# Kernel tuning notes

Hardware: AMD Instinct MI355X
Metric: run time of the kernel (lower is better)

The kernel has to match this reference:

```python
import jax, jax.numpy as jnp
import numpy as np

N = 60000      # n_total_medical_code (graph nodes)
E = 600000     # nnz of sparse adjacency
D = 128        # args.dynamic_size
FEAT = 128     # args.feature_size
B = 256        # len(codeid)
P = 10000      # n_patient
ALPHA = 0.1
EPS = 1e-12    # F.normalize eps


def _l2norm(x):
    # F.normalize(x) : L2 over dim=1
    n = jnp.sqrt(jnp.sum(x * x, axis=1, keepdims=True))
    return x / jnp.maximum(n, EPS)


def _gcn_layer(x, W, edge_row, edge_col, edge_val, init_x):
    # support = X @ W ; out = A @ support (sparse) ; alpha-blend residual ; ReLU
    support = x @ W                                    # [N, D]
    msgs = support[edge_col] * edge_val[:, None]       # [E, D] gather + scale
    agg = jax.ops.segment_sum(msgs, edge_row, num_segments=N)  # [N, D] scatter-add
    out = ALPHA * agg + (1.0 - ALPHA) * init_x
    return jax.nn.relu(out)


def setup_inputs() -> dict:
    key = jax.random.key(0)
    ks = jax.random.split(key, 16)
    stdv = 1.0 / np.sqrt(D)
    in_rnn = D + 1 + FEAT  # 257
    stdv_rnn = 1.0 / np.sqrt(D)
    return {
        "code_dynamic": jax.random.normal(ks[0], (N, D), jnp.float32),
        "init_code_dynamic": jax.random.normal(ks[1], (N, D), jnp.float32),
        "patient_dynamic": jax.random.normal(ks[2], (P, D), jnp.float32),
        "timediffs": jax.random.normal(ks[3], (B, 1), jnp.float32),
        "features": jax.random.normal(ks[4], (B, FEAT), jnp.float32),
        "edge_val": jax.random.uniform(ks[5], (E,), jnp.float32),
        "W1": jax.random.uniform(ks[6], (D, D), jnp.float32, -stdv, stdv),
        "W2": jax.random.uniform(ks[7], (D, D), jnp.float32, -stdv, stdv),
        "W_ih": jax.random.uniform(ks[8], (D, in_rnn), jnp.float32, -stdv_rnn, stdv_rnn),
        "b_ih": jax.random.uniform(ks[9], (D,), jnp.float32, -stdv_rnn, stdv_rnn),
        "W_hh": jax.random.uniform(ks[10], (D, D), jnp.float32, -stdv_rnn, stdv_rnn),
        "b_hh": jax.random.uniform(ks[11], (D,), jnp.float32, -stdv_rnn, stdv_rnn),
        "edge_row": jax.random.randint(ks[12], (E,), 0, N, jnp.int32),
        "edge_col": jax.random.randint(ks[13], (E,), 0, N, jnp.int32),
        "codeid": jax.random.randint(ks[14], (B,), 0, N, jnp.int32),
        "patientid": 0,
    }


def reference(code_dynamic, init_code_dynamic, patient_dynamic, timediffs, features,
              edge_val, W1, W2, W_ih, b_ih, W_hh, b_hh,
              edge_row, edge_col, codeid, patientid):
    # select == 'code_update' branch. x = code_dynamic.clone().detach()
    x = jax.lax.stop_gradient(code_dynamic)
    x = _gcn_layer(x, W1, edge_row, edge_col, edge_val, init_code_dynamic)
    # dropout: inference mode -> identity
    x = _gcn_layer(x, W2, edge_row, edge_col, edge_val, init_code_dynamic)
    code_embed = x[codeid]                               # [B, D]
    patient_embed = jnp.broadcast_to(patient_dynamic[patientid][None, :], (B, D))
    input1 = jnp.concatenate([patient_embed, timediffs, features], axis=1)  # [B, D+1+FEAT]
    # RNNCell (tanh): h' = tanh(x W_ih^T + b_ih + h W_hh^T + b_hh)
    h = jnp.tanh(input1 @ W_ih.T + b_ih + code_embed @ W_hh.T + b_hh)
    return _l2norm(h)
```

## Files before the change

### kernel.cpp

```cpp
#include <hip/hip_runtime.h>
#include <math.h>

#define GD 128
#define ELLW 64
#define NSEG 512

__global__ __launch_bounds__(256) void passA(const int* __restrict__ codeid, int B,
                                             const int* __restrict__ erow,
                                             const int* __restrict__ ecol, int E,
                                             int N, int MAXH,
                                             int* __restrict__ list1,
                                             int* __restrict__ bcnt,
                                             int* __restrict__ cntarr,
                                             const float* __restrict__ patient,
                                             const float* __restrict__ W_ih,
                                             const float* __restrict__ b_ih,
                                             const float* __restrict__ b_hh,
                                             const int* __restrict__ patientid,
                                             float* __restrict__ pc) {
    extern __shared__ unsigned int bm[];
    __shared__ int lcnt;
    int t = threadIdx.x;
    int words = (N + 31) >> 5;
    for (int i = t; i < words; i += 256) bm[i] = 0;
    if (t == 0) lcnt = 0;
    __syncthreads();
    for (int i = t; i < B; i += 256) {
        int c = codeid[i];
        atomicOr(&bm[c >> 5], 1u << (c & 31));
    }
    __syncthreads();

    if (blockIdx.x == gridDim.x - 1 && t < GD) {
        int pid = patientid[0];
        const float* wih = W_ih + (size_t)t * 257;
        const float* pp = patient + (size_t)pid * GD;
        float a0 = 0.f, a1 = 0.f;
#pragma unroll 8
        for (int k = 0; k < GD; k += 2) {
            a0 += pp[k] * wih[k];
            a1 += pp[k + 1] * wih[k + 1];
        }
        pc[t] = b_ih[t] + b_hh[t] + a0 + a1;
    }

    int gid = blockIdx.x * 256 + t, gs = gridDim.x * 256;
    for (int i = gid; i < N; i += gs) cntarr[i] = 0;
    int* seg = list1 + (size_t)blockIdx.x * MAXH;
    for (int e = gid; e < E; e += gs) {
        int r = erow[e];
        if ((bm[r >> 5] >> (r & 31)) & 1u) {
            int idx = atomicAdd(&lcnt, 1);
            seg[idx] = ecol[e];
        }
    }
    __syncthreads();
    if (t == 0) bcnt[blockIdx.x] = lcnt;
}

__global__ __launch_bounds__(256) void passB(const int* __restrict__ erow,
                                             const int* __restrict__ ecol,
                                             const float* __restrict__ ev, int E,
                                             const int* __restrict__ codeid, int B,
                                             const int* __restrict__ list1,
                                             const int* __restrict__ bcnt,
                                             int MAXH, int N,
                                             int* __restrict__ cnt,
                                             int* __restrict__ ellc,
                                             float* __restrict__ ellv) {
    extern __shared__ unsigned int bm[];
    int t = threadIdx.x;
    int words = (N + 31) >> 5;
    for (int i = t; i < words; i += 256) bm[i] = 0;
    __syncthreads();
    for (int i = t; i < B; i += 256) {
        int c = codeid[i];
        atomicOr(&bm[c >> 5], 1u << (c & 31));
    }
    for (int s = t; s < NSEG; s += 256) {
        int c = bcnt[s];
        const int* seg = list1 + (size_t)s * MAXH;
        for (int k = 0; k < c; ++k) {
            int u = seg[k];
            atomicOr(&bm[u >> 5], 1u << (u & 31));
        }
    }
    __syncthreads();

    int gid = blockIdx.x * 256 + t, gs = gridDim.x * 256;
    for (int e = gid; e < E; e += gs) {
        int r = erow[e];
        if ((bm[r >> 5] >> (r & 31)) & 1u) {
            int idx = atomicAdd(&cnt[r], 1);
            if (idx < ELLW) {
                ellc[(size_t)r * ELLW + idx] = ecol[e];
                ellv[(size_t)r * ELLW + idx] = ev[e];
            }
        }
    }
}

__global__ __launch_bounds__(512) void fused12(const float* __restrict__ X,
                                               const float* __restrict__ W1,
                                               const float* __restrict__ W2,
                                               const float* __restrict__ init,
                                               const int* __restrict__ cnt,
                                               const int* __restrict__ ellc,
                                               const float* __restrict__ ellv,
                                               const int* __restrict__ codeid,
                                               const float* __restrict__ timediffs,
                                               const float* __restrict__ features,
                                               const float* __restrict__ W_ih,
                                               const float* __restrict__ W_hh,
                                               const float* __restrict__ pc,
                                               float* __restrict__ out) {
    __shared__ int   sec[ELLW];
    __shared__ float sev[ELLW];
    __shared__ int   ncnt[ELLW];
    __shared__ int   nec[ELLW][ELLW];
    __shared__ float nev[ELLW][ELLW];
    __shared__ float gxs[4][GD];
    __shared__ float p2[4][GD];
    __shared__ float gx2[GD];
    __shared__ float feat[GD];
    __shared__ float ce[GD];
    __shared__ float red[GD];

    int b = blockIdx.x, t = threadIdx.x;
    int sub = t >> 7, j = t & 127;
    int cid = codeid[b];
    int c = cnt[cid]; if (c > ELLW) c = ELLW;

    if (t < c) { sec[t] = ellc[(size_t)cid * ELLW + t]; sev[t] = ellv[(size_t)cid * ELLW + t]; }
    if (t < GD) feat[t] = features[(size_t)b * GD + t];
    __syncthreads();
    if (t < c) { int cc = cnt[sec[t]]; ncnt[t] = cc > ELLW ? ELLW : cc; }
    __syncthreads();
    for (int idx = t; idx < c * ELLW; idx += 512) {
        int i = idx >> 6, k = idx & 63;
        if (k < ncnt[i]) {
            nec[i][k] = ellc[(size_t)sec[i] * ELLW + k];
            nev[i][k] = ellv[(size_t)sec[i] * ELLW + k];
        }
    }
    __syncthreads();

    float a2 = 0.f;
    int nrounds = (c + 3) >> 2;
    for (int ro = 0; ro < nrounds; ++ro) {
        int i = ro * 4 + sub;
        bool act = (i < c);
        if (act) {
            int cc = ncnt[i];
            float g0 = 0.f, g1 = 0.f, g2 = 0.f, g3 = 0.f;
            int k = 0;
            for (; k + 3 < cc; k += 4) {
                g0 += nev[i][k]     * X[(size_t)nec[i][k]     * GD + j];
                g1 += nev[i][k + 1] * X[(size_t)nec[i][k + 1] * GD + j];
                g2 += nev[i][k + 2] * X[(size_t)nec[i][k + 2] * GD + j];
                g3 += nev[i][k + 3] * X[(size_t)nec[i][k + 3] * GD + j];
            }
            for (; k < cc; ++k) g0 += nev[i][k] * X[(size_t)nec[i][k] * GD + j];
            gxs[sub][j] = (g0 + g1) + (g2 + g3);
        }
        __syncthreads();
        if (act) {
            float a0 = 0.f, a1 = 0.f, b2 = 0.f, b3 = 0.f;
            const float* gp = gxs[sub];
#pragma unroll 8
            for (int k = 0; k < GD; k += 4) {
                a0 += gp[k]     * W1[(size_t)k       * GD + j];
                a1 += gp[k + 1] * W1[(size_t)(k + 1) * GD + j];
                b2 += gp[k + 2] * W1[(size_t)(k + 2) * GD + j];
                b3 += gp[k + 3] * W1[(size_t)(k + 3) * GD + j];
            }
            float x1v = fmaxf(0.1f * ((a0 + a1) + (b2 + b3))
                              + 0.9f * init[(size_t)sec[i] * GD + j], 0.f);
            a2 += sev[i] * x1v;
        }
        __syncthreads();
    }
    p2[sub][j] = a2;
    __syncthreads();
    if (t < GD) gx2[t] = (p2[0][t] + p2[1][t]) + (p2[2][t] + p2[3][t]);
    __syncthreads();

    {
        int kb = sub << 5;
        float a0 = 0.f, a1 = 0.f, b2 = 0.f, b3 = 0.f;
#pragma unroll 8
        for (int k = 0; k < 32; k += 4) {
            a0 += gx2[kb + k]     * W2[(size_t)(kb + k)     * GD + j];
            a1 += gx2[kb + k + 1] * W2[(size_t)(kb + k + 1) * GD + j];
            b2 += gx2[kb + k + 2] * W2[(size_t)(kb + k + 2) * GD + j];
            b3 += gx2[kb + k + 3] * W2[(size_t)(kb + k + 3) * GD + j];
        }
        p2[sub][j] = (a0 + a1) + (b2 + b3);
    }
    __syncthreads();
    if (t < GD)
        ce[t] = fmaxf(0.1f * ((p2[0][t] + p2[1][t]) + (p2[2][t] + p2[3][t]))
                      + 0.9f * init[(size_t)cid * GD + t], 0.f);
    __syncthreads();

    {
        const float* wih = W_ih + (size_t)j * 257;
        const float* whh = W_hh + (size_t)j * GD;
        int kb = sub << 5;
        float a0 = (sub == 0) ? (pc[j] + timediffs[b] * wih[GD]) : 0.f;
        float a1 = 0.f;
#pragma unroll 8
        for (int k = 0; k < 32; k += 2) {
            a0 += feat[kb + k]     * wih[129 + kb + k];
            a1 += feat[kb + k + 1] * wih[129 + kb + k + 1];
        }
#pragma unroll 8
        for (int k = 0; k < 32; k += 2) {
            a0 += ce[kb + k]     * whh[kb + k];
            a1 += ce[kb + k + 1] * whh[kb + k + 1];
        }
        p2[sub][j] = a0 + a1;
    }
    __syncthreads();
    float h = 0.f;
    if (t < GD) {
        h = tanhf((p2[0][t] + p2[1][t]) + (p2[2][t] + p2[3][t]));
        red[t] = h * h;
    }
    __syncthreads();
    for (int s = 64; s > 0; s >>= 1) {
        if (t < s) red[t] += red[t + s];
        __syncthreads();
    }
    if (t < GD) {
        float nrm = fmaxf(sqrtf(red[0]), 1e-12f);
        out[(size_t)b * GD + t] = h / nrm;
    }
}


extern "C" void kernel_launch(void* const* d_in, const int* in_sizes, int n_in,
                              void* d_out, int out_size, void* d_ws, size_t ws_size,
                              hipStream_t stream) {
    const float* code_dynamic = (const float*)d_in[0];
    const float* init_cd      = (const float*)d_in[1];
    const float* patient      = (const float*)d_in[2];
    const float* timediffs    = (const float*)d_in[3];
    const float* features     = (const float*)d_in[4];
    const float* edge_val     = (const float*)d_in[5];
    const float* W1           = (const float*)d_in[6];
    const float* W2           = (const float*)d_in[7];
    const float* W_ih         = (const float*)d_in[8];
    const float* b_ih         = (const float*)d_in[9];
    const float* W_hh         = (const float*)d_in[10];
    const float* b_hh         = (const float*)d_in[11];
    const int* edge_row       = (const int*)d_in[12];
    const int* edge_col       = (const int*)d_in[13];
    const int* codeid         = (const int*)d_in[14];
    const int* patientid      = (const int*)d_in[15];

    int N = in_sizes[0] / GD;
    int E = in_sizes[5];
    int B = in_sizes[14];

    int MAXH = 256 * ((E + NSEG * 256 - 1) / (NSEG * 256));

    int*   ellc   = (int*)d_ws;
    float* ellv   = (float*)(ellc + (size_t)N * ELLW);
    int*   cntarr = (int*)(ellv + (size_t)N * ELLW);
    int*   list1  = cntarr + N;
    int*   bcnt   = list1 + (size_t)NSEG * MAXH;
    float* pcbuf  = (float*)(bcnt + NSEG);

    size_t bmBytes = (size_t)((N + 31) / 32) * sizeof(unsigned int);

    passA<<<NSEG, 256, bmBytes, stream>>>(codeid, B, edge_row, edge_col, E,
                                          N, MAXH, list1, bcnt, cntarr,
                                          patient, W_ih, b_ih, b_hh, patientid, pcbuf);
    passB<<<NSEG, 256, bmBytes, stream>>>(edge_row, edge_col, edge_val, E,
                                          codeid, B, list1, bcnt, MAXH, N,
                                          cntarr, ellc, ellv);
    fused12<<<B, 512, 0, stream>>>(code_dynamic, W1, W2, init_cd,
                                   cntarr, ellc, ellv, codeid, timediffs, features,
                                   W_ih, W_hh, pcbuf, (float*)d_out);
}
```

Before: 50.28 us.

## Tile two-hop neighbor gather in groups of eight and share W1 loads

The fused kernel now stages neighbor-of-neighbor ELL lists in chunks of eight first-hop neighbors instead of all 64 at once. This cuts shared memory from roughly 33KB to a few KB, which may raise occupancy. Each 128-thread subgroup handles two neighbors per round, so every W1 load is reused for two dot products and the loop has more independent gathers in flight. Rounds are padded to multiples of four with zero weights, which adds some wasted loads, and an extra barrier per chunk for refilling the lists. The RNN dot products also get four accumulators instead of two.

```diff
diff --git a/kernel.cpp b/kernel.cpp
--- a/kernel.cpp
+++ b/kernel.cpp
@@ -4,6 +4,7 @@
 #define GD 128
 #define ELLW 64
 #define NSEG 512
+#define NT 8
 
 __global__ __launch_bounds__(256) void passA(const int* __restrict__ codeid, int B,
                                              const int* __restrict__ erow,
@@ -116,10 +117,10 @@
                                                float* __restrict__ out) {
     __shared__ int   sec[ELLW];
     __shared__ float sev[ELLW];
-    __shared__ int   ncnt[ELLW];
-    __shared__ int   nec[ELLW][ELLW];
-    __shared__ float nev[ELLW][ELLW];
-    __shared__ float gxs[4][GD];
+    __shared__ int   ncnt[NT];
+    __shared__ int   nec[NT][ELLW];
+    __shared__ float nev[NT][ELLW];
+    __shared__ float gxall[NT][GD];
     __shared__ float p2[4][GD];
     __shared__ float gx2[GD];
     __shared__ float feat[GD];
@@ -134,51 +135,57 @@
     if (t < c) { sec[t] = ellc[(size_t)cid * ELLW + t]; sev[t] = ellv[(size_t)cid * ELLW + t]; }
     if (t < GD) feat[t] = features[(size_t)b * GD + t];
     __syncthreads();
-    if (t < c) { int cc = cnt[sec[t]]; ncnt[t] = cc > ELLW ? ELLW : cc; }
-    __syncthreads();
-    for (int idx = t; idx < c * ELLW; idx += 512) {
-        int i = idx >> 6, k = idx & 63;
-        if (k < ncnt[i]) {
-            nec[i][k] = ellc[(size_t)sec[i] * ELLW + k];
-            nev[i][k] = ellv[(size_t)sec[i] * ELLW + k];
-        }
-    }
-    __syncthreads();
 
     float a2 = 0.f;
-    int nrounds = (c + 3) >> 2;
-    for (int ro = 0; ro < nrounds; ++ro) {
-        int i = ro * 4 + sub;
-        bool act = (i < c);
-        if (act) {
-            int cc = ncnt[i];
-            float g0 = 0.f, g1 = 0.f, g2 = 0.f, g3 = 0.f;
-            int k = 0;
-            for (; k + 3 < cc; k += 4) {
-                g0 += nev[i][k]     * X[(size_t)nec[i][k]     * GD + j];
-                g1 += nev[i][k + 1] * X[(size_t)nec[i][k + 1] * GD + j];
-                g2 += nev[i][k + 2] * X[(size_t)nec[i][k + 2] * GD + j];
-                g3 += nev[i][k + 3] * X[(size_t)nec[i][k + 3] * GD + j];
-            }
-            for (; k < cc; ++k) g0 += nev[i][k] * X[(size_t)nec[i][k] * GD + j];
-            gxs[sub][j] = (g0 + g1) + (g2 + g3);
-        }
-        __syncthreads();
-        if (act) {
-            float a0 = 0.f, a1 = 0.f, b2 = 0.f, b3 = 0.f;
-            const float* gp = gxs[sub];
-#pragma unroll 8
-            for (int k = 0; k < GD; k += 4) {
-                a0 += gp[k]     * W1[(size_t)k       * GD + j];
-                a1 += gp[k + 1] * W1[(size_t)(k + 1) * GD + j];
-                b2 += gp[k + 2] * W1[(size_t)(k + 2) * GD + j];
-                b3 += gp[k + 3] * W1[(size_t)(k + 3) * GD + j];
-            }
-            float x1v = fmaxf(0.1f * ((a0 + a1) + (b2 + b3))
-                              + 0.9f * init[(size_t)sec[i] * GD + j], 0.f);
-            a2 += sev[i] * x1v;
-        }
-        __syncthreads();
+    for (int tb = 0; tb < c; tb += NT) {
+        int nt = c - tb; if (nt > NT) nt = NT;
+        if (t < NT) ncnt[t] = (t < nt) ? min(cnt[sec[tb + t]], ELLW) : 0;
+        __syncthreads();
+        {
+            int i = t >> 6, k = t & 63;
+            bool ok = (k < ncnt[i]);
+            nec[i][k] = ok ? ellc[(size_t)sec[tb + i] * ELLW + k] : 0;
+            nev[i][k] = ok ? ellv[(size_t)sec[tb + i] * ELLW + k] : 0.f;
+        }
+        __syncthreads();
+
+        int ia = sub, ib = sub + 4;
+        int cm = max(ncnt[ia], ncnt[ib]);
+        cm = (cm + 3) & ~3;
+        float ga0 = 0.f, ga1 = 0.f, ga2 = 0.f, ga3 = 0.f;
+        float gb0 = 0.f, gb1 = 0.f, gb2 = 0.f, gb3 = 0.f;
+        for (int k = 0; k < cm; k += 4) {
+            ga0 += nev[ia][k]     * X[(size_t)nec[ia][k]     * GD + j];
+            ga1 += nev[ia][k + 1] * X[(size_t)nec[ia][k + 1] * GD + j];
+            ga2 += nev[ia][k + 2] * X[(size_t)nec[ia][k + 2] * GD + j];
+            ga3 += nev[ia][k + 3] * X[(size_t)nec[ia][k + 3] * GD + j];
+            gb0 += nev[ib][k]     * X[(size_t)nec[ib][k]     * GD + j];
+            gb1 += nev[ib][k + 1] * X[(size_t)nec[ib][k + 1] * GD + j];
+            gb2 += nev[ib][k + 2] * X[(size_t)nec[ib][k + 2] * GD + j];
+            gb3 += nev[ib][k + 3] * X[(size_t)nec[ib][k + 3] * GD + j];
+        }
+        gxall[ia][j] = (ga0 + ga1) + (ga2 + ga3);
+        gxall[ib][j] = (gb0 + gb1) + (gb2 + gb3);
+        __syncthreads();
+
+        float xa0 = 0.f, xa1 = 0.f, xb0 = 0.f, xb1 = 0.f;
+#pragma unroll 4
+        for (int k = 0; k < GD; k += 2) {
+            float w0 = W1[(size_t)k * GD + j];
+            float w1 = W1[(size_t)(k + 1) * GD + j];
+            xa0 += gxall[ia][k] * w0; xa1 += gxall[ia][k + 1] * w1;
+            xb0 += gxall[ib][k] * w0; xb1 += gxall[ib][k + 1] * w1;
+        }
+        if (tb + ia < c) {
+            float x1v = fmaxf(0.1f * (xa0 + xa1)
+                              + 0.9f * init[(size_t)sec[tb + ia] * GD + j], 0.f);
+            a2 += sev[tb + ia] * x1v;
+        }
+        if (tb + ib < c) {
+            float x1v = fmaxf(0.1f * (xb0 + xb1)
+                              + 0.9f * init[(size_t)sec[tb + ib] * GD + j], 0.f);
+            a2 += sev[tb + ib] * x1v;
+        }
     }
     p2[sub][j] = a2;
     __syncthreads();
@@ -208,18 +215,22 @@
         const float* whh = W_hh + (size_t)j * GD;
         int kb = sub << 5;
         float a0 = (sub == 0) ? (pc[j] + timediffs[b] * wih[GD]) : 0.f;
-        float a1 = 0.f;
-#pragma unroll 8
-        for (int k = 0; k < 32; k += 2) {
+        float a1 = 0.f, b2 = 0.f, b3 = 0.f;
+#pragma unroll 8
+        for (int k = 0; k < 32; k += 4) {
             a0 += feat[kb + k]     * wih[129 + kb + k];
             a1 += feat[kb + k + 1] * wih[129 + kb + k + 1];
-        }
-#pragma unroll 8
-        for (int k = 0; k < 32; k += 2) {
+            b2 += feat[kb + k + 2] * wih[129 + kb + k + 2];
+            b3 += feat[kb + k + 3] * wih[129 + kb + k + 3];
+        }
+#pragma unroll 8
+        for (int k = 0; k < 32; k += 4) {
             a0 += ce[kb + k]     * whh[kb + k];
             a1 += ce[kb + k + 1] * whh[kb + k + 1];
-        }
-        p2[sub][j] = a0 + a1;
+            b2 += ce[kb + k + 2] * whh[kb + k + 2];
+            b3 += ce[kb + k + 3] * whh[kb + k + 3];
+        }
+        p2[sub][j] = (a0 + a1) + (b2 + b3);
     }
     __syncthreads();
     float h = 0.f;
```

Measured after the change: 44.41 us. -11.7%, faster.
